# Performance work log

Hardware: AMD Instinct MI355X
Metric: run time of the kernel (lower is better)

## Reference

```python
import jax, jax.numpy as jnp
import numpy as np

NUM_HEAD = 16
DIM = 1024
T, B = 2048, 4


def setup_inputs() -> dict:
    key = jax.random.key(0)
    ks = jax.random.split(key, 12)
    s = 1.0 / np.sqrt(DIM)
    return {
        "x1": jax.random.normal(ks[0], (T, B, DIM), jnp.float32),
        "x2": jax.random.normal(ks[1], (T, B, DIM), jnp.float32),
        "Wq": jax.random.normal(ks[2], (DIM, DIM), jnp.float32) * s,
        "bq": jax.random.normal(ks[3], (DIM,), jnp.float32) * 0.01,
        "Wk": jax.random.normal(ks[4], (DIM, DIM), jnp.float32) * s,
        "bk": jax.random.normal(ks[5], (DIM,), jnp.float32) * 0.01,
        "Wv": jax.random.normal(ks[6], (DIM, DIM), jnp.float32) * s,
        "bv": jax.random.normal(ks[7], (DIM,), jnp.float32) * 0.01,
        "Wu": jax.random.normal(ks[8], (DIM, DIM), jnp.float32) * s,
        "bu": jax.random.normal(ks[9], (DIM,), jnp.float32) * 0.01,
    }


def reference(x1, x2, Wq, bq, Wk, bk, Wv, bv, Wu, bu):
    T1, B1, C = x1.shape
    T2 = x2.shape[0]
    H = NUM_HEAD
    hd = C // H
    # (T,B,C) -> (B,T,C)
    x1b = jnp.transpose(x1, (1, 0, 2))
    x2b = jnp.transpose(x2, (1, 0, 2))
    # torch Linear: y = x @ W.T + b
    q = (x1b @ Wq.T + bq).reshape(B1, T1, H, hd).transpose(0, 2, 1, 3)  # (B,H,T1,hd)
    k = (x2b @ Wk.T + bk).reshape(B1, T2, H, hd).transpose(0, 2, 1, 3)
    v = (x2b @ Wv.T + bv).reshape(B1, T2, H, hd).transpose(0, 2, 1, 3)
    # NOTE: source scales by 1/sqrt(C) (full dim), not 1/sqrt(head_dim)
    attn = jnp.einsum("bhqd,bhkd->bhqk", q, k) / jnp.sqrt(jnp.asarray(C, q.dtype))
    attn = jax.nn.softmax(attn, axis=-1)
    # dropout = identity (eval mode, deterministic reference)
    out = jnp.einsum("bhqk,bhkd->bhqd", attn, v)  # (B,H,T1,hd)
    out = out.transpose(0, 2, 1, 3).reshape(B1, T1, C)  # merge heads
    out = out @ Wu.T + bu
    return out
```

## Files before the change

kernel.cpp:

```cpp
#include <hip/hip_runtime.h>

#define TSEQ 2048
#define BB 4
#define CDIM 1024
#define NH 16
#define HD 64
#define MR (TSEQ*BB)
#define C2SCALE 0.045084220f

typedef __attribute__((ext_vector_type(8))) short sh8;
typedef __attribute__((ext_vector_type(4))) short sh4;
typedef __attribute__((ext_vector_type(4))) float f4;
typedef __attribute__((ext_vector_type(4))) unsigned int u32x4;

__device__ __forceinline__ unsigned short f2bf(float x){
  unsigned u = __builtin_bit_cast(unsigned, x);
  u += 0x7fffu + ((u>>16)&1u);
  return (unsigned short)(u>>16);
}

__device__ __forceinline__ unsigned cvtpk(float a, float b){
  unsigned r;
  asm("v_cvt_pk_bf16_f32 %0, %1, %2" : "=v"(r) : "v"(a), "v"(b));
  return r;
}

__device__ __forceinline__ void gll16(const unsigned short* g, unsigned short* l){
  __builtin_amdgcn_global_load_lds(
      (const __attribute__((address_space(1))) unsigned int*)g,
      (__attribute__((address_space(3))) unsigned int*)l, 16, 0, 0);
}

__global__ void conv_x(const float* __restrict__ a, const float* __restrict__ b,
                       unsigned short* __restrict__ ya, unsigned short* __restrict__ yb){
  const float* s = blockIdx.y ? b : a;
  unsigned short* d = blockIdx.y ? yb : ya;
  int i = (blockIdx.x*256 + threadIdx.x)*4;
  f4 v = *(const f4*)(s+i);
  sh4 o;
  o.x = (short)f2bf(v.x); o.y = (short)f2bf(v.y);
  o.z = (short)f2bf(v.z); o.w = (short)f2bf(v.w);
  *(sh4*)(d+i) = o;
}

__global__ void conv_w(const float* __restrict__ w0, const float* __restrict__ w1,
                       const float* __restrict__ w2, const float* __restrict__ w3,
                       unsigned short* __restrict__ y0, unsigned short* __restrict__ y1,
                       unsigned short* __restrict__ y2, unsigned short* __restrict__ y3){
  const float* s; unsigned short* d;
  switch(blockIdx.y){
    case 0: s=w0; d=y0; break;
    case 1: s=w1; d=y1; break;
    case 2: s=w2; d=y2; break;
    default: s=w3; d=y3; break;
  }
  int i = (blockIdx.x*256 + threadIdx.x)*4;
  f4 v = *(const f4*)(s+i);
  sh4 o;
  o.x = (short)f2bf(v.x); o.y = (short)f2bf(v.y);
  o.z = (short)f2bf(v.z); o.w = (short)f2bf(v.w);
  *(sh4*)(d+i) = o;
}

#define NST 32
#define SLOT 12288

__device__ __forceinline__ void gemm_core(
    const unsigned short* __restrict__ Aglob, const unsigned short* __restrict__ Bglob,
    unsigned short* smem, int m0, int n0, int tid, f4 (&acc)[8][4])
{
  const int wave = tid>>6, lane = tid&63;
  const int g = lane>>4, c = lane&15;
  const int wr = wave>>1, wc = wave&1;

  const unsigned short* aSrc[4]; int aOff[4];
  const unsigned short* bSrc[2]; int bOff[2];
#pragma unroll
  for (int i=0;i<4;i++){
    int slot = i*256+tid; int row = slot>>2, ch = slot&3;
    aSrc[i] = Aglob + (size_t)(m0+row)*CDIM + (ch ^ ((row>>1)&3))*8;
    aOff[i] = slot*8;
  }
#pragma unroll
  for (int i=0;i<2;i++){
    int slot = i*256+tid; int row = slot>>2, ch = slot&3;
    bSrc[i] = Bglob + (size_t)(n0+row)*CDIM + (ch ^ ((row>>1)&3))*8;
    bOff[i] = 8192 + slot*8;
  }
  const int swz = (c>>1)&3;
  const int aro = (wr*128 + c)*32 + (g ^ swz)*8;
  const int bro = 8192 + (wc*64 + c)*32 + (g ^ swz)*8;

#pragma unroll
  for (int i=0;i<4;i++) gll16(aSrc[i],    smem + aOff[i]);
#pragma unroll
  for (int i=0;i<2;i++) gll16(bSrc[i],    smem + bOff[i]);
#pragma unroll
  for (int i=0;i<4;i++) gll16(aSrc[i]+32, smem + SLOT + aOff[i]);
#pragma unroll
  for (int i=0;i<2;i++) gll16(bSrc[i]+32, smem + SLOT + bOff[i]);
  asm volatile("s_waitcnt vmcnt(6)" ::: "memory");
  __builtin_amdgcn_s_barrier();

  int q = 0;
  for (int s=0; s<NST; s++){
    unsigned short* bufc = smem + q*SLOT;
    int rr = q+2; if (rr>=3) rr-=3;
    unsigned short* dst = smem + rr*SLOT;
    if (s+2 < NST){
      const int ko = (s+2)*32;
#pragma unroll
      for (int i=0;i<4;i++) gll16(aSrc[i]+ko, dst + aOff[i]);
#pragma unroll
      for (int i=0;i<2;i++) gll16(bSrc[i]+ko, dst + bOff[i]);
    }
    sh8 af[8], bfr[4];
#pragma unroll
    for (int mt=0;mt<8;mt++) af[mt]  = *(const sh8*)(bufc + aro + mt*512);
#pragma unroll
    for (int nt=0;nt<4;nt++) bfr[nt] = *(const sh8*)(bufc + bro + nt*512);
    __builtin_amdgcn_s_setprio(1);
#pragma unroll
    for (int mt=0;mt<8;mt++)
#pragma unroll
      for (int nt=0;nt<4;nt++)
        acc[mt][nt] = __builtin_amdgcn_mfma_f32_16x16x32_bf16(af[mt], bfr[nt], acc[mt][nt],0,0,0);
    __builtin_amdgcn_s_setprio(0);
    if (s < NST-2)       asm volatile("s_waitcnt vmcnt(6)" ::: "memory");
    else if (s == NST-2) asm volatile("s_waitcnt vmcnt(0)" ::: "memory");
    __builtin_amdgcn_s_barrier();
    q = (q==2)?0:q+1;
  }
}

__global__ __launch_bounds__(256,2) void gemm_u(
    const unsigned short* __restrict__ A, const unsigned short* __restrict__ Bw,
    const float* __restrict__ bias, float* __restrict__ Cout){
  __shared__ unsigned short smem[3*SLOT];
  const int tid  = threadIdx.x;
  const int wave = tid>>6, lane = tid&63;
  const int g = lane>>4, c = lane&15;
  const int m0 = blockIdx.x*256, n0 = blockIdx.y*128;
  const int wr = wave>>1, wc = wave&1;
  f4 acc[8][4] = {};
  gemm_core(A, Bw, smem, m0, n0, tid, acc);

#pragma unroll
  for (int nt=0; nt<4; nt++){
    int nn = n0 + wc*64 + nt*16 + c;
    float bsv = bias[nn];
#pragma unroll
    for (int mt=0; mt<8; mt++){
      int mb = m0 + wr*128 + mt*16 + 4*g;
#pragma unroll
      for (int r=0; r<4; r++)
        Cout[(size_t)(mb+r)*CDIM + nn] = acc[mt][nt][r] + bsv;
    }
  }
}

__global__ __launch_bounds__(256,2) void gemm_qkv(
    const unsigned short* __restrict__ x1b, const unsigned short* __restrict__ x2b,
    const unsigned short* __restrict__ wq, const unsigned short* __restrict__ wk,
    const unsigned short* __restrict__ wv,
    const float* __restrict__ bq, const float* __restrict__ bk, const float* __restrict__ bv,
    unsigned short* __restrict__ Qo, unsigned short* __restrict__ Ko,
    unsigned short* __restrict__ Vo){
  __shared__ unsigned short smem[3*SLOT];
  const int z = blockIdx.z;
  const unsigned short* A  = (z==0) ? x1b : x2b;
  const unsigned short* Bw = (z==0) ? wq : (z==1) ? wk : wv;
  const float* bias        = (z==0) ? bq : (z==1) ? bk : bv;
  const int tid  = threadIdx.x;
  const int wave = tid>>6, lane = tid&63;
  const int g = lane>>4, c = lane&15;
  const int m0 = blockIdx.x*256, n0 = blockIdx.y*128;
  const int wr = wave>>1, wc = wave&1;
  f4 acc[8][4] = {};
  gemm_core(A, Bw, smem, m0, n0, tid, acc);

#pragma unroll
  for (int nt=0; nt<4; nt++){
    int nn = n0 + wc*64 + nt*16 + c;
    float bsv = bias[nn];
#pragma unroll
    for (int mt=0; mt<8; mt++){
      int mb = m0 + wr*128 + mt*16 + 4*g;
#pragma unroll
      for (int r=0; r<4; r++){
        float v = acc[mt][nt][r] + bsv;
        int mm = mb + r;
        if (z==0){
          Qo[(size_t)mm*CDIM + nn] = f2bf(v*C2SCALE);
        } else if (z==1){
          Ko[(size_t)mm*CDIM + nn] = f2bf(v);
        } else {
          int t = mm>>2, bb = mm&3, h = nn>>6, d = nn&63;
          Vo[(((size_t)bb*NH + h)*HD + d)*TSEQ + t] = f2bf(v);
        }
      }
    }
  }
}

__global__ __launch_bounds__(256,4) void attn_kernel(
    const unsigned short* __restrict__ Q, const unsigned short* __restrict__ Kb,
    const unsigned short* __restrict__ Vt, unsigned short* __restrict__ O){
  __shared__ unsigned short Ks[2][64*64];
  __shared__ unsigned short Vs[2][64*64];
  const int tid=threadIdx.x, wave=tid>>6, lane=tid&63;
  const int g=lane>>4, c=lane&15;
  const bool godd = (g&1);
  const int gx = blockIdx.x;
  const int bh = ((gx>>7)<<3) | (gx&7);
  const int qt = (gx>>3)&15;
  const int b = bh>>4, h = bh&15;
  const int qbase = qt*128 + wave*32;

  const unsigned short* kb0[2];
  const unsigned short* vb0[2];
#pragma unroll
  for (int i=0; i<2; i++){
    int cc = i*256+tid;
    int krow = cc>>3, kch = (cc&7) ^ (krow&7);
    kb0[i] = Kb + ((size_t)krow*BB + b)*CDIM + h*HD + kch*8;
    int vd = cc>>3, vch = (cc&7) ^ (vd&7);
    vb0[i] = Vt + ((size_t)(b*NH+h)*HD + vd)*TSEQ + vch*8;
  }

  sh8 qfr[2][2];
#pragma unroll
  for (int qf=0; qf<2; qf++)
#pragma unroll
    for (int kc=0; kc<2; kc++){
      int t = qbase + qf*16 + c;
      qfr[qf][kc] = *(const sh8*)(Q + ((size_t)t*BB + b)*CDIM + h*HD + kc*32 + g*8);
    }

  f4 oacc[4][2] = {};
  float lrun[2] = {0.f, 0.f};

#pragma unroll
  for (int i=0; i<2; i++){
    gll16(kb0[i], Ks[0] + (i*256+tid)*8);
    gll16(vb0[i], Vs[0] + (i*256+tid)*8);
  }
  __syncthreads();

  const int NT = TSEQ/64;
  int cur = 0;
  for (int it=0; it<NT; it++){
    if (it+1 < NT){
      int k0n = (it+1)*64;
#pragma unroll
      for (int i=0; i<2; i++){
        gll16(kb0[i] + (size_t)k0n*BB*CDIM, Ks[cur^1] + (i*256+tid)*8);
        gll16(vb0[i] + k0n,                 Vs[cur^1] + (i*256+tid)*8);
      }
    }
    const unsigned short* ks = Ks[cur];
    const unsigned short* vs = Vs[cur];

#pragma unroll
    for (int sub=0; sub<2; sub++){
      f4 sacc[2][2] = {};
      __builtin_amdgcn_s_setprio(1);
#pragma unroll
      for (int j=0; j<2; j++){
        int kf = sub*2 + j;
        sh8 af[2];
#pragma unroll
        for (int kc=0; kc<2; kc++){
          int ch = (kc*4+g) ^ (c&7);
          af[kc] = *(const sh8*)(ks + (kf*16+c)*64 + ch*8);
        }
#pragma unroll
        for (int kc=0; kc<2; kc++)
#pragma unroll
          for (int qf=0; qf<2; qf++)
            sacc[j][qf] = __builtin_amdgcn_mfma_f32_16x16x32_bf16(af[kc], qfr[qf][kc], sacc[j][qf],0,0,0);
      }
      __builtin_amdgcn_s_setprio(0);

      sh8 pf[2];
#pragma unroll
      for (int qf=0; qf<2; qf++){
        f4 sa = sacc[0][qf];
        f4 sb = sacc[1][qf];
        float pa0 = __builtin_amdgcn_exp2f(sa[0]);
        float pa1 = __builtin_amdgcn_exp2f(sa[1]);
        float pa2 = __builtin_amdgcn_exp2f(sa[2]);
        float pa3 = __builtin_amdgcn_exp2f(sa[3]);
        float pb0 = __builtin_amdgcn_exp2f(sb[0]);
        float pb1 = __builtin_amdgcn_exp2f(sb[1]);
        float pb2 = __builtin_amdgcn_exp2f(sb[2]);
        float pb3 = __builtin_amdgcn_exp2f(sb[3]);
        lrun[qf] += ((pa0+pa1)+(pa2+pa3)) + ((pb0+pb1)+(pb2+pb3));
        unsigned A0 = cvtpk(pa0, pa1);
        unsigned A1 = cvtpk(pa2, pa3);
        unsigned B0 = cvtpk(pb0, pb1);
        unsigned B1 = cvtpk(pb2, pb3);
        asm("v_permlane32_swap_b32 %0, %1" : "+v"(A0), "+v"(B0));
        asm("v_permlane32_swap_b32 %0, %1" : "+v"(A1), "+v"(B1));
        unsigned xA0 = (unsigned)__builtin_amdgcn_ds_swizzle((int)A0, 0x401F);
        unsigned xA1 = (unsigned)__builtin_amdgcn_ds_swizzle((int)A1, 0x401F);
        unsigned xB0 = (unsigned)__builtin_amdgcn_ds_swizzle((int)B0, 0x401F);
        unsigned xB1 = (unsigned)__builtin_amdgcn_ds_swizzle((int)B1, 0x401F);
        u32x4 pw;
        pw.x = godd ? xB0 : A0;
        pw.y = godd ? xB1 : A1;
        pw.z = godd ? B0  : xA0;
        pw.w = godd ? B1  : xA1;
        pf[qf] = __builtin_bit_cast(sh8, pw);
      }
      __builtin_amdgcn_s_setprio(1);
#pragma unroll
      for (int df=0; df<4; df++){
        int ch = (sub*4+g) ^ (c&7);
        sh8 vf = *(const sh8*)(vs + (df*16+c)*64 + ch*8);
#pragma unroll
        for (int qf=0; qf<2; qf++)
          oacc[df][qf] = __builtin_amdgcn_mfma_f32_16x16x32_bf16(vf, pf[qf], oacc[df][qf],0,0,0);
      }
      __builtin_amdgcn_s_setprio(0);
    }

    __syncthreads();
    cur ^= 1;
  }

#pragma unroll
  for (int qf=0; qf<2; qf++){
    lrun[qf] += __shfl_xor(lrun[qf], 16, 64);
    lrun[qf] += __shfl_xor(lrun[qf], 32, 64);
    float inv = 1.0f/lrun[qf];
    int t = qbase + qf*16 + c;
#pragma unroll
    for (int df=0; df<4; df++){
      uint2 pr;
      pr.x = cvtpk(oacc[df][qf][0]*inv, oacc[df][qf][1]*inv);
      pr.y = cvtpk(oacc[df][qf][2]*inv, oacc[df][qf][3]*inv);
      *(uint2*)(O + ((size_t)b*TSEQ + t)*CDIM + h*HD + df*16 + 4*g) = pr;
    }
  }
}

extern "C" void kernel_launch(void* const* d_in, const int* in_sizes, int n_in,
                              void* d_out, int out_size, void* d_ws, size_t ws_size,
                              hipStream_t stream){
  (void)in_sizes; (void)n_in; (void)out_size; (void)ws_size;
  const float* x1 = (const float*)d_in[0];
  const float* x2 = (const float*)d_in[1];
  const float* Wq = (const float*)d_in[2];
  const float* bq = (const float*)d_in[3];
  const float* Wk = (const float*)d_in[4];
  const float* bk = (const float*)d_in[5];
  const float* Wv = (const float*)d_in[6];
  const float* bv = (const float*)d_in[7];
  const float* Wu = (const float*)d_in[8];
  const float* bu = (const float*)d_in[9];

  unsigned short* ws = (unsigned short*)d_ws;
  size_t o = 0;
  unsigned short* x1b = ws + o; o += (size_t)MR*CDIM;
  unsigned short* x2b = ws + o; o += (size_t)MR*CDIM;
  unsigned short* wqb = ws + o; o += (size_t)CDIM*CDIM;
  unsigned short* wkb = ws + o; o += (size_t)CDIM*CDIM;
  unsigned short* wvb = ws + o; o += (size_t)CDIM*CDIM;
  unsigned short* wub = ws + o; o += (size_t)CDIM*CDIM;
  unsigned short* Qb  = ws + o; o += (size_t)MR*CDIM;
  unsigned short* Kbf = ws + o; o += (size_t)MR*CDIM;
  unsigned short* Vtb = ws + o; o += (size_t)MR*CDIM;
  unsigned short* Ob  = x1b;

  conv_x<<<dim3((MR*CDIM)/1024, 2),   256, 0, stream>>>(x1, x2, x1b, x2b);
  conv_w<<<dim3((CDIM*CDIM)/1024, 4), 256, 0, stream>>>(Wq, Wk, Wv, Wu, wqb, wkb, wvb, wub);

  gemm_qkv<<<dim3(MR/256, CDIM/128, 3), 256, 0, stream>>>(
      x1b, x2b, wqb, wkb, wvb, bq, bk, bv, Qb, Kbf, Vtb);
  attn_kernel<<<dim3(1024), 256, 0, stream>>>(Qb, Kbf, Vtb, Ob);
  gemm_u<<<dim3(MR/256, CDIM/128), 256, 0, stream>>>(Ob, wub, bu, (float*)d_out);
}
```

Before: 318.5 us.

## Use 256x256 GEMM tiles with 8 waves and fine-grained K=64 double buffering

The QKV and output-projection GEMMs move from 256x128 tiles on 4 waves to 256x256 tiles on 8 waves (512 threads). Each K step now covers 64 elements instead of 32, using two LDS buffers instead of three, with a new XOR swizzle. Global-to-LDS prefetches are split into quarters and interleaved with MFMA phases between barriers. The aim is more operand reuse per byte loaded and better overlap of loads with compute, at the cost of 128KB LDS per block, more barriers per K step, and half as many blocks in the grid.

```diff
diff --git a/kernel.cpp b/kernel.cpp
--- a/kernel.cpp
+++ b/kernel.cpp
@@ -62,92 +62,104 @@
   *(sh4*)(d+i) = o;
 }
 
-#define NST 32
-#define SLOT 12288
+#define NKT 16
+#define TBUF 32768
 
 __device__ __forceinline__ void gemm_core(
     const unsigned short* __restrict__ Aglob, const unsigned short* __restrict__ Bglob,
     unsigned short* smem, int m0, int n0, int tid, f4 (&acc)[8][4])
 {
-  const int wave = tid>>6, lane = tid&63;
+  const int lane = tid&63;
   const int g = lane>>4, c = lane&15;
-  const int wr = wave>>1, wc = wave&1;
-
-  const unsigned short* aSrc[4]; int aOff[4];
-  const unsigned short* bSrc[2]; int bOff[2];
-#pragma unroll
-  for (int i=0;i<4;i++){
-    int slot = i*256+tid; int row = slot>>2, ch = slot&3;
-    aSrc[i] = Aglob + (size_t)(m0+row)*CDIM + (ch ^ ((row>>1)&3))*8;
-    aOff[i] = slot*8;
-  }
-#pragma unroll
-  for (int i=0;i<2;i++){
-    int slot = i*256+tid; int row = slot>>2, ch = slot&3;
-    bSrc[i] = Bglob + (size_t)(n0+row)*CDIM + (ch ^ ((row>>1)&3))*8;
-    bOff[i] = 8192 + slot*8;
-  }
-  const int swz = (c>>1)&3;
-  const int aro = (wr*128 + c)*32 + (g ^ swz)*8;
-  const int bro = 8192 + (wc*64 + c)*32 + (g ^ swz)*8;
-
-#pragma unroll
-  for (int i=0;i<4;i++) gll16(aSrc[i],    smem + aOff[i]);
-#pragma unroll
-  for (int i=0;i<2;i++) gll16(bSrc[i],    smem + bOff[i]);
-#pragma unroll
-  for (int i=0;i<4;i++) gll16(aSrc[i]+32, smem + SLOT + aOff[i]);
-#pragma unroll
-  for (int i=0;i<2;i++) gll16(bSrc[i]+32, smem + SLOT + bOff[i]);
+  const int wv = tid>>6;
+  const int wr = wv>>2, wcn = wv&3;
+
+  const int rloc = tid>>3, cho = tid&7;
+  const int aside = (rloc>>5)<<7;
+  const int ar = (rloc&31) + aside;
+  const int schk = (cho ^ (rloc&7))*8;
+  const unsigned short* aS = Aglob + (size_t)(m0+ar)*CDIM + schk;
+  const unsigned short* bS = Bglob + (size_t)(n0+rloc)*CDIM + schk;
+  const int aD = ar*64 + cho*8;
+  const int bD = 16384 + rloc*64 + cho*8;
+
+#define STA(k2,q) gll16(aS + (size_t)(q)*32*CDIM + (k2)*64, smem + ((k2)&1)*TBUF + (q)*2048 + aD)
+#define STB(k2,q) gll16(bS + (size_t)(q)*64*CDIM + (k2)*64, smem + ((k2)&1)*TBUF + (q)*4096 + bD)
+
+  const int ch0 = (g ^ (c&7))*8;
+  const int ch1 = ((4+g) ^ (c&7))*8;
+  const int arow0 = (wr*128 + c)*64;
+  const int brow0 = 16384 + (wcn*64 + c)*64;
+
+#pragma unroll
+  for (int q=0;q<4;q++) STA(0,q);
+#pragma unroll
+  for (int q=0;q<4;q++) STB(0,q);
+#pragma unroll
+  for (int q=0;q<3;q++){ STA(1,q); STB(1,q); }
   asm volatile("s_waitcnt vmcnt(6)" ::: "memory");
   __builtin_amdgcn_s_barrier();
 
-  int q = 0;
-  for (int s=0; s<NST; s++){
-    unsigned short* bufc = smem + q*SLOT;
-    int rr = q+2; if (rr>=3) rr-=3;
-    unsigned short* dst = smem + rr*SLOT;
-    if (s+2 < NST){
-      const int ko = (s+2)*32;
-#pragma unroll
-      for (int i=0;i<4;i++) gll16(aSrc[i]+ko, dst + aOff[i]);
-#pragma unroll
-      for (int i=0;i<2;i++) gll16(bSrc[i]+ko, dst + bOff[i]);
-    }
-    sh8 af[8], bfr[4];
-#pragma unroll
-    for (int mt=0;mt<8;mt++) af[mt]  = *(const sh8*)(bufc + aro + mt*512);
-#pragma unroll
-    for (int nt=0;nt<4;nt++) bfr[nt] = *(const sh8*)(bufc + bro + nt*512);
-    __builtin_amdgcn_s_setprio(1);
-#pragma unroll
-    for (int mt=0;mt<8;mt++)
-#pragma unroll
-      for (int nt=0;nt<4;nt++)
-        acc[mt][nt] = __builtin_amdgcn_mfma_f32_16x16x32_bf16(af[mt], bfr[nt], acc[mt][nt],0,0,0);
-    __builtin_amdgcn_s_setprio(0);
-    if (s < NST-2)       asm volatile("s_waitcnt vmcnt(6)" ::: "memory");
-    else if (s == NST-2) asm volatile("s_waitcnt vmcnt(0)" ::: "memory");
-    __builtin_amdgcn_s_barrier();
-    q = (q==2)?0:q+1;
-  }
-}
-
-__global__ __launch_bounds__(256,2) void gemm_u(
+  for (int kt=0; kt<NKT; kt++){
+    const unsigned short* bufA = smem + (kt&1)*TBUF;
+    sh8 bfr[4][2];
+#pragma unroll
+    for (int p=0; p<4; p++){
+      sh8 af[2][2];
+#pragma unroll
+      for (int i=0;i<2;i++){
+        af[i][0] = *(const sh8*)(bufA + arow0 + (2*p+i)*1024 + ch0);
+        af[i][1] = *(const sh8*)(bufA + arow0 + (2*p+i)*1024 + ch1);
+      }
+      if (p==0){
+#pragma unroll
+        for (int nt=0;nt<4;nt++){
+          bfr[nt][0] = *(const sh8*)(bufA + brow0 + nt*1024 + ch0);
+          bfr[nt][1] = *(const sh8*)(bufA + brow0 + nt*1024 + ch1);
+        }
+      }
+      if (p==0){
+        if (kt+1 < NKT){ STA(kt+1,3); STB(kt+1,3); }
+      } else {
+        if (kt+2 < NKT){ STA(kt+2,p-1); STB(kt+2,p-1); }
+      }
+      __builtin_amdgcn_s_barrier();
+      __builtin_amdgcn_s_setprio(1);
+#pragma unroll
+      for (int i=0;i<2;i++)
+#pragma unroll
+        for (int nt=0;nt<4;nt++){
+          acc[2*p+i][nt] = __builtin_amdgcn_mfma_f32_16x16x32_bf16(af[i][0], bfr[nt][0], acc[2*p+i][nt],0,0,0);
+          acc[2*p+i][nt] = __builtin_amdgcn_mfma_f32_16x16x32_bf16(af[i][1], bfr[nt][1], acc[2*p+i][nt],0,0,0);
+        }
+      __builtin_amdgcn_s_setprio(0);
+      if (p==3){
+        if (kt < NKT-2)       asm volatile("s_waitcnt vmcnt(6)" ::: "memory");
+        else if (kt == NKT-2) asm volatile("s_waitcnt vmcnt(0)" ::: "memory");
+      }
+      __builtin_amdgcn_s_barrier();
+    }
+  }
+#undef STA
+#undef STB
+}
+
+__global__ __launch_bounds__(512,2) void gemm_u(
     const unsigned short* __restrict__ A, const unsigned short* __restrict__ Bw,
     const float* __restrict__ bias, float* __restrict__ Cout){
-  __shared__ unsigned short smem[3*SLOT];
+  __shared__ unsigned short smem[2*TBUF];
   const int tid  = threadIdx.x;
-  const int wave = tid>>6, lane = tid&63;
+  const int lane = tid&63;
   const int g = lane>>4, c = lane&15;
-  const int m0 = blockIdx.x*256, n0 = blockIdx.y*128;
-  const int wr = wave>>1, wc = wave&1;
+  const int wv = tid>>6;
+  const int wr = wv>>2, wcn = wv&3;
+  const int m0 = blockIdx.x*256, n0 = blockIdx.y*256;
   f4 acc[8][4] = {};
   gemm_core(A, Bw, smem, m0, n0, tid, acc);
 
 #pragma unroll
   for (int nt=0; nt<4; nt++){
-    int nn = n0 + wc*64 + nt*16 + c;
+    int nn = n0 + wcn*64 + nt*16 + c;
     float bsv = bias[nn];
 #pragma unroll
     for (int mt=0; mt<8; mt++){
@@ -159,29 +171,30 @@
   }
 }
 
-__global__ __launch_bounds__(256,2) void gemm_qkv(
+__global__ __launch_bounds__(512,2) void gemm_qkv(
     const unsigned short* __restrict__ x1b, const unsigned short* __restrict__ x2b,
     const unsigned short* __restrict__ wq, const unsigned short* __restrict__ wk,
     const unsigned short* __restrict__ wv,
     const float* __restrict__ bq, const float* __restrict__ bk, const float* __restrict__ bv,
     unsigned short* __restrict__ Qo, unsigned short* __restrict__ Ko,
     unsigned short* __restrict__ Vo){
-  __shared__ unsigned short smem[3*SLOT];
+  __shared__ unsigned short smem[2*TBUF];
   const int z = blockIdx.z;
   const unsigned short* A  = (z==0) ? x1b : x2b;
   const unsigned short* Bw = (z==0) ? wq : (z==1) ? wk : wv;
   const float* bias        = (z==0) ? bq : (z==1) ? bk : bv;
   const int tid  = threadIdx.x;
-  const int wave = tid>>6, lane = tid&63;
+  const int lane = tid&63;
   const int g = lane>>4, c = lane&15;
-  const int m0 = blockIdx.x*256, n0 = blockIdx.y*128;
-  const int wr = wave>>1, wc = wave&1;
+  const int wv2 = tid>>6;
+  const int wr = wv2>>2, wcn = wv2&3;
+  const int m0 = blockIdx.x*256, n0 = blockIdx.y*256;
   f4 acc[8][4] = {};
   gemm_core(A, Bw, smem, m0, n0, tid, acc);
 
 #pragma unroll
   for (int nt=0; nt<4; nt++){
-    int nn = n0 + wc*64 + nt*16 + c;
+    int nn = n0 + wcn*64 + nt*16 + c;
     float bsv = bias[nn];
 #pragma unroll
     for (int mt=0; mt<8; mt++){
@@ -376,8 +389,8 @@
   conv_x<<<dim3((MR*CDIM)/1024, 2),   256, 0, stream>>>(x1, x2, x1b, x2b);
   conv_w<<<dim3((CDIM*CDIM)/1024, 4), 256, 0, stream>>>(Wq, Wk, Wv, Wu, wqb, wkb, wvb, wub);
 
-  gemm_qkv<<<dim3(MR/256, CDIM/128, 3), 256, 0, stream>>>(
+  gemm_qkv<<<dim3(MR/256, CDIM/256, 3), 512, 0, stream>>>(
       x1b, x2b, wqb, wkb, wvb, bq, bk, bv, Qb, Kbf, Vtb);
   attn_kernel<<<dim3(1024), 256, 0, stream>>>(Qb, Kbf, Vtb, Ob);
-  gemm_u<<<dim3(MR/256, CDIM/128), 256, 0, stream>>>(Ob, wub, bu, (float*)d_out);
-}
+  gemm_u<<<dim3(MR/256, CDIM/256), 512, 0, stream>>>(Ob, wub, bu, (float*)d_out);
+}
```

Result: slower. 333.4 us (+4.7%).
